# Kernel tuning notes

Measured on AMD Instinct MI355X. Metric: run time of the kernel, lower is better.

## Reference

```python
import jax, jax.numpy as jnp
import numpy as np

EPS = 1e-06

def elu_feature_map(x):
    return jax.nn.elu(x) + 1.0

def setup_inputs() -> dict:
    key = jax.random.key(0)
    kq, kk, kv = jax.random.split(key, 3)
    N, L, S, H, D = 8, 8192, 8192, 8, 32
    queries = jax.random.normal(kq, (N, L, H, D), dtype=jnp.float32)
    keys = jax.random.normal(kk, (N, S, H, D), dtype=jnp.float32)
    values = jax.random.normal(kv, (N, S, H, D), dtype=jnp.float32)
    return {"queries": queries, "keys": keys, "values": values}

def reference(queries, keys, values):
    # Linear attention: phi(Q) (phi(K)^T V) normalized by phi(Q) . sum(phi(K))
    Q = elu_feature_map(queries)            # [N, L, H, D]
    K = elu_feature_map(keys)               # [N, S, H, D]
    v_length = values.shape[1]
    v = values / v_length                   # [N, S, H, Dv]
    KV = jnp.einsum('nshd,nshv->nhdv', K, v)           # [N, H, D, Dv]
    Z = 1.0 / (jnp.einsum('nlhd,nhd->nlh', Q, K.sum(axis=1)) + EPS)  # [N, L, H]
    out = jnp.einsum('nlhd,nhdv->nlhv', Q, KV) * Z[..., None] * v_length
    return out
```

## Files before the change

kernel.cpp:

```cpp
#include <hip/hip_runtime.h>
#include <hip/hip_bf16.h>


#define N_      8
#define L_      8192
#define S_      8192
#define H_      8
#define D_      32
#define NH_     64
#define CH1_    16
#define SPC1_   512
#define STR1_   36
#define KVE_    (D_ * D_)
#define PKS_    (KVE_ + D_)

typedef short short8 __attribute__((ext_vector_type(8)));
typedef float f32x4  __attribute__((ext_vector_type(4)));

__device__ __forceinline__ float phi_f(float x) {
    return x > 0.f ? x + 1.f : __expf(x);
}

__device__ __forceinline__ unsigned short bf16_bits(float x) {
    __hip_bfloat16 h = __float2bfloat16(x);
    unsigned short u;
    __builtin_memcpy(&u, &h, 2);
    return u;
}

__device__ __forceinline__ void split_bf16(float x, short& hi, short& lo) {
    __hip_bfloat16 hb = __float2bfloat16(x);
    const float xh = __bfloat162float(hb);
    __hip_bfloat16 lb = __float2bfloat16(x - xh);
    __builtin_memcpy(&hi, &hb, 2);
    __builtin_memcpy(&lo, &lb, 2);
}

template <bool ATOMIC>
__global__ __launch_bounds__(256) void la_phase1(
    const float* __restrict__ keys, const float* __restrict__ values,
    float* __restrict__ outp )
{
    __shared__ unsigned kS[2][32][STR1_];
    __shared__ unsigned vS[2][32][STR1_];
    __shared__ float red_ks[4][8][4];
    const int nh = blockIdx.x, chunk = blockIdx.y;
    const int n = nh >> 3, h = nh & 7;
    const int t = threadIdx.x, lane = t & 63, w = t >> 6;
    const int row8 = t >> 3;
    const int c4   = t & 7;
    const int row_l = lane & 15, kg = lane >> 4;
    const int dt = w >> 1, vt = w & 1;
    const int odd = row8 & 1;
    const int dv0 = (c4 << 2) + (odd ? 2 : 0);
    const int s2lo = row8 >> 1;
    const float* kb = keys   + ((size_t)n * S_) * 256 + h * 32 + (c4 << 2);
    const float* vb = values + ((size_t)n * S_) * 256 + h * 32 + (c4 << 2);
    const int s0 = chunk * SPC1_;

    float ks4[4] = {0.f, 0.f, 0.f, 0.f};
    f32x4 cacc = {0.f, 0.f, 0.f, 0.f};
    float4 Lka, Lkb, Lva, Lvb;

    auto LOADT = [&](int tb) {
        const size_t g0 = ((size_t)(s0 + (tb << 6) + row8)) << 8;
        const size_t g1 = ((size_t)(s0 + (tb << 6) + row8 + 32)) << 8;
        Lka = *(const float4*)(kb + g0);
        Lkb = *(const float4*)(kb + g1);
        Lva = *(const float4*)(vb + g0);
        Lvb = *(const float4*)(vb + g1);
    };
    auto STORE4 = [&](unsigned (*Sarr)[STR1_], const unsigned short* x, int s2) {
        const unsigned mA = (unsigned)x[0] | ((unsigned)x[1] << 16);
        const unsigned mB = (unsigned)x[2] | ((unsigned)x[3] << 16);
        const unsigned pA = __shfl_xor(mA, 8);
        const unsigned pB = __shfl_xor(mB, 8);
        const unsigned m = odd ? mB : mA, p = odd ? pB : pA;
        const unsigned se = odd ? p : m;
        const unsigned so = odd ? m : p;
        const unsigned w0 = (se & 0xffffu) | ((so & 0xffffu) << 16);
        const unsigned w1 = (se >> 16) | (so & 0xffff0000u);
        Sarr[dv0][4 * ((s2 >> 2) ^ (dv0 >> 3)) + (s2 & 3)]           = w0;
        Sarr[dv0 + 1][4 * ((s2 >> 2) ^ ((dv0 + 1) >> 3)) + (s2 & 3)] = w1;
    };
    auto PROCT = [&](int buf) {
        const float f0[4] = {phi_f(Lka.x), phi_f(Lka.y), phi_f(Lka.z), phi_f(Lka.w)};
        const float f1[4] = {phi_f(Lkb.x), phi_f(Lkb.y), phi_f(Lkb.z), phi_f(Lkb.w)};
        unsigned short kx[4], ky[4], vx[4], vy[4];
#pragma unroll
        for (int j = 0; j < 4; ++j) ks4[j] += f0[j] + f1[j];
        kx[0] = bf16_bits(f0[0]); kx[1] = bf16_bits(f0[1]);
        kx[2] = bf16_bits(f0[2]); kx[3] = bf16_bits(f0[3]);
        ky[0] = bf16_bits(f1[0]); ky[1] = bf16_bits(f1[1]);
        ky[2] = bf16_bits(f1[2]); ky[3] = bf16_bits(f1[3]);
        vx[0] = bf16_bits(Lva.x); vx[1] = bf16_bits(Lva.y);
        vx[2] = bf16_bits(Lva.z); vx[3] = bf16_bits(Lva.w);
        vy[0] = bf16_bits(Lvb.x); vy[1] = bf16_bits(Lvb.y);
        vy[2] = bf16_bits(Lvb.z); vy[3] = bf16_bits(Lvb.w);
        STORE4(kS[buf], kx, s2lo);
        STORE4(kS[buf], ky, s2lo + 16);
        STORE4(vS[buf], vx, s2lo);
        STORE4(vS[buf], vy, s2lo + 16);
    };
    auto FRAG = [&](const unsigned (*Sarr)[STR1_], int row, int sh) -> short8 {
        const int g = ((sh << 2) | kg) ^ (row >> 3);
        union { uint4 u; short8 s; } U;
        U.u = *(const uint4*)&Sarr[row][g << 2];
        return U.s;
    };
    auto COMPT = [&](int buf) {
#pragma unroll
        for (int sh = 0; sh < 2; ++sh) {
            const short8 A = FRAG(kS[buf], (dt << 4) + row_l, sh);
            const short8 B = FRAG(vS[buf], (vt << 4) + row_l, sh);
            cacc = __builtin_amdgcn_mfma_f32_16x16x32_bf16(A, B, cacc, 0, 0, 0);
        }
    };

    LOADT(0);
    PROCT(0);
    __syncthreads();
#pragma unroll
    for (int tb = 0; tb < 8; ++tb) {
        const int cur = tb & 1;
        if (tb < 7) LOADT(tb + 1);
        COMPT(cur);
        if (tb < 7) PROCT(cur ^ 1);
        __syncthreads();
    }

#pragma unroll
    for (int j = 0; j < 4; ++j) {
        float x = ks4[j];
        x += __shfl_xor(x, 8);
        x += __shfl_xor(x, 16);
        x += __shfl_xor(x, 32);
        ks4[j] = x;
    }
    if (lane < 8) {
#pragma unroll
        for (int j = 0; j < 4; ++j) red_ks[w][lane][j] = ks4[j];
    }
    __syncthreads();

    if (ATOMIC) {
        float* p = outp + (size_t)nh * PKS_;
#pragma unroll
        for (int r = 0; r < 4; ++r) {
            const int dd = (dt << 4) + (kg << 2) + r;
            const int vv = (vt << 4) + row_l;
            atomicAdd(&p[dd * D_ + vv], cacc[r]);
        }
        if (t < 32) {
            const float s = red_ks[0][t >> 2][t & 3] + red_ks[1][t >> 2][t & 3]
                          + red_ks[2][t >> 2][t & 3] + red_ks[3][t >> 2][t & 3];
            atomicAdd(&p[KVE_ + t], s);
        }
    } else {
        float* p = outp + ((size_t)nh * CH1_ + chunk) * PKS_;
#pragma unroll
        for (int r = 0; r < 4; ++r) {
            const int dd = (dt << 4) + (kg << 2) + r;
            const int vv = (vt << 4) + row_l;
            p[dd * D_ + vv] = cacc[r];
        }
        if (t < 32) {
            p[KVE_ + t] = red_ks[0][t >> 2][t & 3] + red_ks[1][t >> 2][t & 3]
                        + red_ks[2][t >> 2][t & 3] + red_ks[3][t >> 2][t & 3];
        }
    }
}

__global__ __launch_bounds__(256) void la_reduce(
    const float* __restrict__ partials,
    short* __restrict__ kvThi, short* __restrict__ kvTlo,
    float* __restrict__ ksumf)
{
    const int nh = blockIdx.x;
    for (int e = threadIdx.x; e < PKS_; e += 256) {
        const float* p = partials + (size_t)nh * CH1_ * PKS_ + e;
        float s = 0.f;
#pragma unroll
        for (int c = 0; c < CH1_; ++c) s += p[(size_t)c * PKS_];
        if (e < KVE_) {
            const int d = e >> 5, v = e & 31;
            short hi, lo; split_bf16(s, hi, lo);
            kvThi[nh * KVE_ + v * D_ + d] = hi;
            kvTlo[nh * KVE_ + v * D_ + d] = lo;
        } else {
            ksumf[nh * D_ + (e - KVE_)] = s;
        }
    }
}

__global__ __launch_bounds__(256) void la_convert(
    const float* __restrict__ kvf,
    short* __restrict__ kvThi, short* __restrict__ kvTlo,
    float* __restrict__ ksumf)
{
    const int nh = blockIdx.x;
    for (int e = threadIdx.x; e < PKS_; e += 256) {
        const float s = kvf[(size_t)nh * PKS_ + e];
        if (e < KVE_) {
            const int d = e >> 5, v = e & 31;
            short hi, lo; split_bf16(s, hi, lo);
            kvThi[nh * KVE_ + v * D_ + d] = hi;
            kvTlo[nh * KVE_ + v * D_ + d] = lo;
        } else {
            ksumf[nh * D_ + (e - KVE_)] = s;
        }
    }
}

__global__ void la_zero(float* __restrict__ p, int nelem) {
    const int i = blockIdx.x * 256 + threadIdx.x;
    if (i < nelem) p[i] = 0.f;
}

__global__ __launch_bounds__(256) void la_phase2(
    const float* __restrict__ queries,
    const short* __restrict__ kvThi, const short* __restrict__ kvTlo,
    const float* __restrict__ ksumf, float* __restrict__ out)
{
    const int t = threadIdx.x, lane = t & 63, w = t >> 6;
    const int wt = blockIdx.x * 4 + w;
    const int h  = wt & 7;
    const int rt = wt >> 3;
    const size_t rowg0 = (size_t)rt * 16;
    const int n = (int)(rowg0 >> 13);
    const int nh = n * 8 + h;
    const int row_l = lane & 15;
    const int kg    = lane >> 4;

    const float* qp = queries + (rowg0 + row_l) * 256 + h * D_ + kg * 8;
    float qa[8];
    {
        const float4 qA = *(const float4*)(qp);
        const float4 qB = *(const float4*)(qp + 4);
        qa[0] = phi_f(qA.x); qa[1] = phi_f(qA.y); qa[2] = phi_f(qA.z); qa[3] = phi_f(qA.w);
        qa[4] = phi_f(qB.x); qa[5] = phi_f(qB.y); qa[6] = phi_f(qB.z); qa[7] = phi_f(qB.w);
    }
    short8 ahi, alo;
#pragma unroll
    for (int e = 0; e < 8; ++e) {
        short hs, ls; split_bf16(qa[e], hs, ls);
        ahi[e] = hs; alo[e] = ls;
    }

    const short* bh = kvThi + (size_t)nh * KVE_;
    const short* bl = kvTlo + (size_t)nh * KVE_;
    const short8 bh0 = *(const short8*)(bh + (row_l     ) * D_ + kg * 8);
    const short8 bh1 = *(const short8*)(bh + (row_l + 16) * D_ + kg * 8);
    const short8 bl0 = *(const short8*)(bl + (row_l     ) * D_ + kg * 8);
    const short8 bl1 = *(const short8*)(bl + (row_l + 16) * D_ + kg * 8);

    f32x4 c0 = {0.f, 0.f, 0.f, 0.f}, c1 = {0.f, 0.f, 0.f, 0.f};
    c0 = __builtin_amdgcn_mfma_f32_16x16x32_bf16(alo, bh0, c0, 0, 0, 0);
    c0 = __builtin_amdgcn_mfma_f32_16x16x32_bf16(ahi, bl0, c0, 0, 0, 0);
    c0 = __builtin_amdgcn_mfma_f32_16x16x32_bf16(ahi, bh0, c0, 0, 0, 0);
    c1 = __builtin_amdgcn_mfma_f32_16x16x32_bf16(alo, bh1, c1, 0, 0, 0);
    c1 = __builtin_amdgcn_mfma_f32_16x16x32_bf16(ahi, bl1, c1, 0, 0, 0);
    c1 = __builtin_amdgcn_mfma_f32_16x16x32_bf16(ahi, bh1, c1, 0, 0, 0);

    const float* ksp = ksumf + nh * D_ + kg * 8;
    float dt;
    {
        const float4 kA = *(const float4*)(ksp);
        const float4 kB = *(const float4*)(ksp + 4);
        dt = qa[0] * kA.x;
        dt = fmaf(qa[1], kA.y, dt); dt = fmaf(qa[2], kA.z, dt);
        dt = fmaf(qa[3], kA.w, dt); dt = fmaf(qa[4], kB.x, dt);
        dt = fmaf(qa[5], kB.y, dt); dt = fmaf(qa[6], kB.z, dt);
        dt = fmaf(qa[7], kB.w, dt);
    }
    dt += __shfl_xor(dt, 16);
    dt += __shfl_xor(dt, 32);

    float* ob = out + rowg0 * 256 + h * D_ + row_l;
#pragma unroll
    for (int r = 0; r < 4; ++r) {
        const int rowp = kg * 4 + r;
        const float drow = __shfl(dt, rowp);
        const float z = __builtin_amdgcn_rcpf(drow + 1e-6f);
        ob[(size_t)rowp * 256]      = c0[r] * z;
        ob[(size_t)rowp * 256 + 16] = c1[r] * z;
    }
}

extern "C" void kernel_launch(void* const* d_in, const int* in_sizes, int n_in,
                              void* d_out, int out_size, void* d_ws, size_t ws_size,
                              hipStream_t stream)
{
    const float* queries = (const float*)d_in[0];
    const float* keys    = (const float*)d_in[1];
    const float* values  = (const float*)d_in[2];
    float* out = (float*)d_out;
    float* ws  = (float*)d_ws;

    const size_t partial_elems = (size_t)NH_ * CH1_ * PKS_;
    const size_t split_elems   = (size_t)NH_ * KVE_;
    const size_t split_floats  = split_elems / 2;
    const size_t ksum_floats   = (size_t)NH_ * D_;
    const dim3 blk(256);
    const int p2_blocks = (N_ * L_ * H_) / 16 / 4;

    if (ws_size >= (partial_elems + 2 * split_floats + ksum_floats) * sizeof(float)) {
        float* partials = ws;
        short* kvThi = (short*)(ws + partial_elems);
        short* kvTlo = kvThi + split_elems;
        float* ksumf = (float*)(kvTlo + split_elems);
        la_phase1<false><<<dim3(NH_, CH1_), blk, 0, stream>>>(keys, values, partials);
        la_reduce<<<dim3(NH_), blk, 0, stream>>>(partials, kvThi, kvTlo, ksumf);
        la_phase2<<<dim3(p2_blocks), blk, 0, stream>>>(queries, kvThi, kvTlo, ksumf, out);
    } else {
        float* kvf = ws;
        short* kvThi = (short*)(ws + (size_t)NH_ * PKS_);
        short* kvTlo = kvThi + split_elems;
        float* ksumf = (float*)(kvTlo + split_elems);
        const int nz = (int)((size_t)NH_ * PKS_);
        la_zero<<<dim3((nz + 255) / 256), blk, 0, stream>>>(kvf, nz);
        la_phase1<true><<<dim3(NH_, CH1_), blk, 0, stream>>>(keys, values, kvf);
        la_convert<<<dim3(NH_), blk, 0, stream>>>(kvf, kvThi, kvTlo, ksumf);
        la_phase2<<<dim3(p2_blocks), blk, 0, stream>>>(queries, kvThi, kvTlo, ksumf, out);
    }
}
```

Before: 62.97 us.

## Process eight row tiles per wave in phase2, reusing KV fragments and prefetching queries

Phase 2 now gives each block a fixed (n,h) pair and makes each wave loop over eight 16-row tiles. The split-bf16 KV fragments and the key-sum are loaded once per wave and reused across those tiles. The next tile's query loads are issued before the current tile's MFMA and normalisation work, a software prefetch. The grid shrinks from 8192 blocks to 1024, which cuts launch and per-wave setup costs but lowers parallelism and could leave less latency hiding on the memory-bound output stores.

```diff
diff --git a/kernel.cpp b/kernel.cpp
--- a/kernel.cpp
+++ b/kernel.cpp
@@ -223,67 +223,71 @@
     const float* __restrict__ ksumf, float* __restrict__ out)
 {
     const int t = threadIdx.x, lane = t & 63, w = t >> 6;
-    const int wt = blockIdx.x * 4 + w;
-    const int h  = wt & 7;
-    const int rt = wt >> 3;
-    const size_t rowg0 = (size_t)rt * 16;
-    const int n = (int)(rowg0 >> 13);
-    const int nh = n * 8 + h;
+    const int bx = blockIdx.x;
+    const int nh = bx & 63;
+    const int g  = bx >> 6;
+    const int n = nh >> 3, h = nh & 7;
     const int row_l = lane & 15;
     const int kg    = lane >> 4;
 
-    const float* qp = queries + (rowg0 + row_l) * 256 + h * D_ + kg * 8;
-    float qa[8];
-    {
-        const float4 qA = *(const float4*)(qp);
-        const float4 qB = *(const float4*)(qp + 4);
-        qa[0] = phi_f(qA.x); qa[1] = phi_f(qA.y); qa[2] = phi_f(qA.z); qa[3] = phi_f(qA.w);
-        qa[4] = phi_f(qB.x); qa[5] = phi_f(qB.y); qa[6] = phi_f(qB.z); qa[7] = phi_f(qB.w);
-    }
-    short8 ahi, alo;
-#pragma unroll
-    for (int e = 0; e < 8; ++e) {
-        short hs, ls; split_bf16(qa[e], hs, ls);
-        ahi[e] = hs; alo[e] = ls;
-    }
-
-    const short* bh = kvThi + (size_t)nh * KVE_;
-    const short* bl = kvTlo + (size_t)nh * KVE_;
-    const short8 bh0 = *(const short8*)(bh + (row_l     ) * D_ + kg * 8);
-    const short8 bh1 = *(const short8*)(bh + (row_l + 16) * D_ + kg * 8);
-    const short8 bl0 = *(const short8*)(bl + (row_l     ) * D_ + kg * 8);
-    const short8 bl1 = *(const short8*)(bl + (row_l + 16) * D_ + kg * 8);
-
-    f32x4 c0 = {0.f, 0.f, 0.f, 0.f}, c1 = {0.f, 0.f, 0.f, 0.f};
-    c0 = __builtin_amdgcn_mfma_f32_16x16x32_bf16(alo, bh0, c0, 0, 0, 0);
-    c0 = __builtin_amdgcn_mfma_f32_16x16x32_bf16(ahi, bl0, c0, 0, 0, 0);
-    c0 = __builtin_amdgcn_mfma_f32_16x16x32_bf16(ahi, bh0, c0, 0, 0, 0);
-    c1 = __builtin_amdgcn_mfma_f32_16x16x32_bf16(alo, bh1, c1, 0, 0, 0);
-    c1 = __builtin_amdgcn_mfma_f32_16x16x32_bf16(ahi, bl1, c1, 0, 0, 0);
-    c1 = __builtin_amdgcn_mfma_f32_16x16x32_bf16(ahi, bh1, c1, 0, 0, 0);
-
-    const float* ksp = ksumf + nh * D_ + kg * 8;
-    float dt;
-    {
-        const float4 kA = *(const float4*)(ksp);
-        const float4 kB = *(const float4*)(ksp + 4);
-        dt = qa[0] * kA.x;
+    const short* bhp = kvThi + (size_t)nh * KVE_;
+    const short* blp = kvTlo + (size_t)nh * KVE_;
+    const short8 bh0 = *(const short8*)(bhp + (row_l     ) * D_ + kg * 8);
+    const short8 bh1 = *(const short8*)(bhp + (row_l + 16) * D_ + kg * 8);
+    const short8 bl0 = *(const short8*)(blp + (row_l     ) * D_ + kg * 8);
+    const short8 bl1 = *(const short8*)(blp + (row_l + 16) * D_ + kg * 8);
+    const float4 kA = *(const float4*)(ksumf + nh * D_ + kg * 8);
+    const float4 kB = *(const float4*)(ksumf + nh * D_ + kg * 8 + 4);
+
+    const size_t row0 = ((size_t)n << 13) + ((size_t)(g * 4 + w) << 7);
+    const float* qbase = queries + (row0 + row_l) * 256 + h * D_ + kg * 8;
+    float* obase = out + row0 * 256 + h * D_ + row_l;
+
+    float4 qA = *(const float4*)(qbase);
+    float4 qB = *(const float4*)(qbase + 4);
+
+#pragma unroll
+    for (int tt = 0; tt < 8; ++tt) {
+        const float4 cA = qA, cB = qB;
+        if (tt < 7) {
+            const float* qp = qbase + (size_t)(tt + 1) * 16 * 256;
+            qA = *(const float4*)(qp);
+            qB = *(const float4*)(qp + 4);
+        }
+        float qa[8];
+        qa[0] = phi_f(cA.x); qa[1] = phi_f(cA.y); qa[2] = phi_f(cA.z); qa[3] = phi_f(cA.w);
+        qa[4] = phi_f(cB.x); qa[5] = phi_f(cB.y); qa[6] = phi_f(cB.z); qa[7] = phi_f(cB.w);
+        short8 ahi, alo;
+#pragma unroll
+        for (int e = 0; e < 8; ++e) {
+            short hs, ls; split_bf16(qa[e], hs, ls);
+            ahi[e] = hs; alo[e] = ls;
+        }
+        f32x4 c0 = {0.f, 0.f, 0.f, 0.f}, c1 = {0.f, 0.f, 0.f, 0.f};
+        c0 = __builtin_amdgcn_mfma_f32_16x16x32_bf16(alo, bh0, c0, 0, 0, 0);
+        c0 = __builtin_amdgcn_mfma_f32_16x16x32_bf16(ahi, bl0, c0, 0, 0, 0);
+        c0 = __builtin_amdgcn_mfma_f32_16x16x32_bf16(ahi, bh0, c0, 0, 0, 0);
+        c1 = __builtin_amdgcn_mfma_f32_16x16x32_bf16(alo, bh1, c1, 0, 0, 0);
+        c1 = __builtin_amdgcn_mfma_f32_16x16x32_bf16(ahi, bl1, c1, 0, 0, 0);
+        c1 = __builtin_amdgcn_mfma_f32_16x16x32_bf16(ahi, bh1, c1, 0, 0, 0);
+
+        float dt = qa[0] * kA.x;
         dt = fmaf(qa[1], kA.y, dt); dt = fmaf(qa[2], kA.z, dt);
         dt = fmaf(qa[3], kA.w, dt); dt = fmaf(qa[4], kB.x, dt);
         dt = fmaf(qa[5], kB.y, dt); dt = fmaf(qa[6], kB.z, dt);
         dt = fmaf(qa[7], kB.w, dt);
-    }
-    dt += __shfl_xor(dt, 16);
-    dt += __shfl_xor(dt, 32);
-
-    float* ob = out + rowg0 * 256 + h * D_ + row_l;
-#pragma unroll
-    for (int r = 0; r < 4; ++r) {
-        const int rowp = kg * 4 + r;
-        const float drow = __shfl(dt, rowp);
-        const float z = __builtin_amdgcn_rcpf(drow + 1e-6f);
-        ob[(size_t)rowp * 256]      = c0[r] * z;
-        ob[(size_t)rowp * 256 + 16] = c1[r] * z;
+        dt += __shfl_xor(dt, 16);
+        dt += __shfl_xor(dt, 32);
+
+        float* ob = obase + (size_t)tt * 16 * 256;
+#pragma unroll
+        for (int r = 0; r < 4; ++r) {
+            const int rowp = kg * 4 + r;
+            const float drow = __shfl(dt, rowp);
+            const float z = __builtin_amdgcn_rcpf(drow + 1e-6f);
+            ob[(size_t)rowp * 256]      = c0[r] * z;
+            ob[(size_t)rowp * 256 + 16] = c1[r] * z;
+        }
     }
 }
 
@@ -302,7 +306,7 @@
     const size_t split_floats  = split_elems / 2;
     const size_t ksum_floats   = (size_t)NH_ * D_;
     const dim3 blk(256);
-    const int p2_blocks = (N_ * L_ * H_) / 16 / 4;
+    const int p2_blocks = 1024;
 
     if (ws_size >= (partial_elems + 2 * split_floats + ksum_floats) * sizeof(float)) {
         float* partials = ws;
```

After: 70.10 us. 11.3% more time.

## Process two row tiles per wave in phase2 and swizzle block order

Applied to the files above, without the earlier changes.

Each wave in la_phase2 now handles 32 query rows instead of 16. The KV bf16 split fragments and ksum are loaded once and reused across both row tiles, and both tiles' query loads are issued up front. The grid is halved, and a block-index swizzle remaps blocks across 8 groups, likely to spread neighbouring blocks over XCDs or L2. This cuts redundant KV loads and per-wave overhead, at the cost of half as many waves and more register pressure.

```diff
diff --git a/kernel.cpp b/kernel.cpp
--- a/kernel.cpp
+++ b/kernel.cpp
@@ -223,29 +223,18 @@
     const float* __restrict__ ksumf, float* __restrict__ out)
 {
     const int t = threadIdx.x, lane = t & 63, w = t >> 6;
-    const int wt = blockIdx.x * 4 + w;
-    const int h  = wt & 7;
-    const int rt = wt >> 3;
-    const size_t rowg0 = (size_t)rt * 16;
-    const int n = (int)(rowg0 >> 13);
+    const int bx0 = blockIdx.x;
+    const int px  = bx0 >> 1;
+    const int swz = (px & 7) * 256 + (px >> 3);
+    const int bx  = (swz << 1) | (bx0 & 1);
+    const int wt  = bx * 4 + w;
+    const int h   = wt & 7;
+    const int rt2 = wt >> 3;
+    const size_t rowg0 = (size_t)rt2 * 32;
+    const int n  = (int)(rowg0 >> 13);
     const int nh = n * 8 + h;
     const int row_l = lane & 15;
     const int kg    = lane >> 4;
-
-    const float* qp = queries + (rowg0 + row_l) * 256 + h * D_ + kg * 8;
-    float qa[8];
-    {
-        const float4 qA = *(const float4*)(qp);
-        const float4 qB = *(const float4*)(qp + 4);
-        qa[0] = phi_f(qA.x); qa[1] = phi_f(qA.y); qa[2] = phi_f(qA.z); qa[3] = phi_f(qA.w);
-        qa[4] = phi_f(qB.x); qa[5] = phi_f(qB.y); qa[6] = phi_f(qB.z); qa[7] = phi_f(qB.w);
-    }
-    short8 ahi, alo;
-#pragma unroll
-    for (int e = 0; e < 8; ++e) {
-        short hs, ls; split_bf16(qa[e], hs, ls);
-        ahi[e] = hs; alo[e] = ls;
-    }
 
     const short* bh = kvThi + (size_t)nh * KVE_;
     const short* bl = kvTlo + (size_t)nh * KVE_;
@@ -253,37 +242,57 @@
     const short8 bh1 = *(const short8*)(bh + (row_l + 16) * D_ + kg * 8);
     const short8 bl0 = *(const short8*)(bl + (row_l     ) * D_ + kg * 8);
     const short8 bl1 = *(const short8*)(bl + (row_l + 16) * D_ + kg * 8);
-
-    f32x4 c0 = {0.f, 0.f, 0.f, 0.f}, c1 = {0.f, 0.f, 0.f, 0.f};
-    c0 = __builtin_amdgcn_mfma_f32_16x16x32_bf16(alo, bh0, c0, 0, 0, 0);
-    c0 = __builtin_amdgcn_mfma_f32_16x16x32_bf16(ahi, bl0, c0, 0, 0, 0);
-    c0 = __builtin_amdgcn_mfma_f32_16x16x32_bf16(ahi, bh0, c0, 0, 0, 0);
-    c1 = __builtin_amdgcn_mfma_f32_16x16x32_bf16(alo, bh1, c1, 0, 0, 0);
-    c1 = __builtin_amdgcn_mfma_f32_16x16x32_bf16(ahi, bl1, c1, 0, 0, 0);
-    c1 = __builtin_amdgcn_mfma_f32_16x16x32_bf16(ahi, bh1, c1, 0, 0, 0);
-
-    const float* ksp = ksumf + nh * D_ + kg * 8;
-    float dt;
-    {
-        const float4 kA = *(const float4*)(ksp);
-        const float4 kB = *(const float4*)(ksp + 4);
-        dt = qa[0] * kA.x;
+    const float4 kA = *(const float4*)(ksumf + nh * D_ + kg * 8);
+    const float4 kB = *(const float4*)(ksumf + nh * D_ + kg * 8 + 4);
+
+    const float* qp0 = queries + (rowg0 + row_l) * 256 + h * D_ + kg * 8;
+    const float* qp1 = qp0 + 16 * 256;
+    float4 qA[2], qB[2];
+    qA[0] = *(const float4*)(qp0);
+    qB[0] = *(const float4*)(qp0 + 4);
+    qA[1] = *(const float4*)(qp1);
+    qB[1] = *(const float4*)(qp1 + 4);
+
+    float* ob0 = out + rowg0 * 256 + h * D_ + row_l;
+
+#pragma unroll
+    for (int tt = 0; tt < 2; ++tt) {
+        float qa[8];
+        qa[0] = phi_f(qA[tt].x); qa[1] = phi_f(qA[tt].y);
+        qa[2] = phi_f(qA[tt].z); qa[3] = phi_f(qA[tt].w);
+        qa[4] = phi_f(qB[tt].x); qa[5] = phi_f(qB[tt].y);
+        qa[6] = phi_f(qB[tt].z); qa[7] = phi_f(qB[tt].w);
+        short8 ahi, alo;
+#pragma unroll
+        for (int e = 0; e < 8; ++e) {
+            short hs, ls; split_bf16(qa[e], hs, ls);
+            ahi[e] = hs; alo[e] = ls;
+        }
+        f32x4 c0 = {0.f, 0.f, 0.f, 0.f}, c1 = {0.f, 0.f, 0.f, 0.f};
+        c0 = __builtin_amdgcn_mfma_f32_16x16x32_bf16(alo, bh0, c0, 0, 0, 0);
+        c0 = __builtin_amdgcn_mfma_f32_16x16x32_bf16(ahi, bl0, c0, 0, 0, 0);
+        c0 = __builtin_amdgcn_mfma_f32_16x16x32_bf16(ahi, bh0, c0, 0, 0, 0);
+        c1 = __builtin_amdgcn_mfma_f32_16x16x32_bf16(alo, bh1, c1, 0, 0, 0);
+        c1 = __builtin_amdgcn_mfma_f32_16x16x32_bf16(ahi, bl1, c1, 0, 0, 0);
+        c1 = __builtin_amdgcn_mfma_f32_16x16x32_bf16(ahi, bh1, c1, 0, 0, 0);
+
+        float dt = qa[0] * kA.x;
         dt = fmaf(qa[1], kA.y, dt); dt = fmaf(qa[2], kA.z, dt);
         dt = fmaf(qa[3], kA.w, dt); dt = fmaf(qa[4], kB.x, dt);
         dt = fmaf(qa[5], kB.y, dt); dt = fmaf(qa[6], kB.z, dt);
         dt = fmaf(qa[7], kB.w, dt);
-    }
-    dt += __shfl_xor(dt, 16);
-    dt += __shfl_xor(dt, 32);
-
-    float* ob = out + rowg0 * 256 + h * D_ + row_l;
-#pragma unroll
-    for (int r = 0; r < 4; ++r) {
-        const int rowp = kg * 4 + r;
-        const float drow = __shfl(dt, rowp);
-        const float z = __builtin_amdgcn_rcpf(drow + 1e-6f);
-        ob[(size_t)rowp * 256]      = c0[r] * z;
-        ob[(size_t)rowp * 256 + 16] = c1[r] * z;
+        dt += __shfl_xor(dt, 16);
+        dt += __shfl_xor(dt, 32);
+
+        float* ob = ob0 + (size_t)tt * 16 * 256;
+#pragma unroll
+        for (int r = 0; r < 4; ++r) {
+            const int rowp = kg * 4 + r;
+            const float drow = __shfl(dt, rowp);
+            const float z = __builtin_amdgcn_rcpf(drow + 1e-6f);
+            ob[(size_t)rowp * 256]      = c0[r] * z;
+            ob[(size_t)rowp * 256 + 16] = c1[r] * z;
+        }
     }
 }
 
@@ -302,7 +311,7 @@
     const size_t split_floats  = split_elems / 2;
     const size_t ksum_floats   = (size_t)NH_ * D_;
     const dim3 blk(256);
-    const int p2_blocks = (N_ * L_ * H_) / 16 / 4;
+    const int p2_blocks = (N_ * L_ * H_) / 32 / 4;
 
     if (ws_size >= (partial_elems + 2 * split_floats + ksum_floats) * sizeof(float)) {
         float* partials = ws;
```

Measured after the change: 66.75 us. 1.06x slower.

## Stage phase-2 query rows through swizzled LDS with 512-thread blocks

Applied to the files above, without the earlier changes.

Phase 2 now uses one 512-thread block per 16 rows, one wave per head. Each block loads the full 16x256 query rows into shared memory with coalesced float4 reads, applying phi on the way and an XOR swizzle to avoid bank conflicts. Each wave then reads its head slice from LDS. This replaces the earlier strided per-wave 32-byte global reads with fully contiguous row loads, at the cost of 16KB of LDS per block and a block barrier.

```diff
diff --git a/kernel.cpp b/kernel.cpp
--- a/kernel.cpp
+++ b/kernel.cpp
@@ -217,34 +217,31 @@
     if (i < nelem) p[i] = 0.f;
 }
 
-__global__ __launch_bounds__(256) void la_phase2(
+__global__ __launch_bounds__(512) void la_phase2(
     const float* __restrict__ queries,
     const short* __restrict__ kvThi, const short* __restrict__ kvTlo,
     const float* __restrict__ ksumf, float* __restrict__ out)
 {
+    __shared__ float qs[16 * 256];
     const int t = threadIdx.x, lane = t & 63, w = t >> 6;
-    const int wt = blockIdx.x * 4 + w;
-    const int h  = wt & 7;
-    const int rt = wt >> 3;
-    const size_t rowg0 = (size_t)rt * 16;
-    const int n = (int)(rowg0 >> 13);
+    const size_t rowg0 = (size_t)blockIdx.x * 16;
+    const int n  = (int)(rowg0 >> 13);
+    const int h  = w;
     const int nh = n * 8 + h;
     const int row_l = lane & 15;
     const int kg    = lane >> 4;
 
-    const float* qp = queries + (rowg0 + row_l) * 256 + h * D_ + kg * 8;
-    float qa[8];
     {
-        const float4 qA = *(const float4*)(qp);
-        const float4 qB = *(const float4*)(qp + 4);
-        qa[0] = phi_f(qA.x); qa[1] = phi_f(qA.y); qa[2] = phi_f(qA.z); qa[3] = phi_f(qA.w);
-        qa[4] = phi_f(qB.x); qa[5] = phi_f(qB.y); qa[6] = phi_f(qB.z); qa[7] = phi_f(qB.w);
-    }
-    short8 ahi, alo;
-#pragma unroll
-    for (int e = 0; e < 8; ++e) {
-        short hs, ls; split_bf16(qa[e], hs, ls);
-        ahi[e] = hs; alo[e] = ls;
+        const int row = t & 15, seg = t >> 4;
+        const float* qp = queries + (rowg0 + row) * 256 + seg * 8;
+        const float4 a = *(const float4*)(qp);
+        const float4 b = *(const float4*)(qp + 4);
+        const int p0 = ((seg << 1) | 0) ^ (row & 7);
+        const int p1 = ((seg << 1) | 1) ^ (row & 7);
+        *(float4*)&qs[row * 256 + p0 * 4] =
+            make_float4(phi_f(a.x), phi_f(a.y), phi_f(a.z), phi_f(a.w));
+        *(float4*)&qs[row * 256 + p1 * 4] =
+            make_float4(phi_f(b.x), phi_f(b.y), phi_f(b.z), phi_f(b.w));
     }
 
     const short* bh = kvThi + (size_t)nh * KVE_;
@@ -253,6 +250,26 @@
     const short8 bh1 = *(const short8*)(bh + (row_l + 16) * D_ + kg * 8);
     const short8 bl0 = *(const short8*)(bl + (row_l     ) * D_ + kg * 8);
     const short8 bl1 = *(const short8*)(bl + (row_l + 16) * D_ + kg * 8);
+    const float4 kA = *(const float4*)(ksumf + nh * D_ + kg * 8);
+    const float4 kB = *(const float4*)(ksumf + nh * D_ + kg * 8 + 4);
+
+    __syncthreads();
+
+    float qa[8];
+    {
+        const int g0 = (h * 8 + kg * 2)     ^ (row_l & 7);
+        const int g1 = (h * 8 + kg * 2 + 1) ^ (row_l & 7);
+        const float4 f0 = *(const float4*)&qs[row_l * 256 + g0 * 4];
+        const float4 f1 = *(const float4*)&qs[row_l * 256 + g1 * 4];
+        qa[0] = f0.x; qa[1] = f0.y; qa[2] = f0.z; qa[3] = f0.w;
+        qa[4] = f1.x; qa[5] = f1.y; qa[6] = f1.z; qa[7] = f1.w;
+    }
+    short8 ahi, alo;
+#pragma unroll
+    for (int e = 0; e < 8; ++e) {
+        short hs, ls; split_bf16(qa[e], hs, ls);
+        ahi[e] = hs; alo[e] = ls;
+    }
 
     f32x4 c0 = {0.f, 0.f, 0.f, 0.f}, c1 = {0.f, 0.f, 0.f, 0.f};
     c0 = __builtin_amdgcn_mfma_f32_16x16x32_bf16(alo, bh0, c0, 0, 0, 0);
@@ -262,17 +279,11 @@
     c1 = __builtin_amdgcn_mfma_f32_16x16x32_bf16(ahi, bl1, c1, 0, 0, 0);
     c1 = __builtin_amdgcn_mfma_f32_16x16x32_bf16(ahi, bh1, c1, 0, 0, 0);
 
-    const float* ksp = ksumf + nh * D_ + kg * 8;
-    float dt;
-    {
-        const float4 kA = *(const float4*)(ksp);
-        const float4 kB = *(const float4*)(ksp + 4);
-        dt = qa[0] * kA.x;
-        dt = fmaf(qa[1], kA.y, dt); dt = fmaf(qa[2], kA.z, dt);
-        dt = fmaf(qa[3], kA.w, dt); dt = fmaf(qa[4], kB.x, dt);
-        dt = fmaf(qa[5], kB.y, dt); dt = fmaf(qa[6], kB.z, dt);
-        dt = fmaf(qa[7], kB.w, dt);
-    }
+    float dt = qa[0] * kA.x;
+    dt = fmaf(qa[1], kA.y, dt); dt = fmaf(qa[2], kA.z, dt);
+    dt = fmaf(qa[3], kA.w, dt); dt = fmaf(qa[4], kB.x, dt);
+    dt = fmaf(qa[5], kB.y, dt); dt = fmaf(qa[6], kB.z, dt);
+    dt = fmaf(qa[7], kB.w, dt);
     dt += __shfl_xor(dt, 16);
     dt += __shfl_xor(dt, 32);
 
@@ -302,7 +313,8 @@
     const size_t split_floats  = split_elems / 2;
     const size_t ksum_floats   = (size_t)NH_ * D_;
     const dim3 blk(256);
-    const int p2_blocks = (N_ * L_ * H_) / 16 / 4;
+    const dim3 blk2(512);
+    const int p2_blocks = (N_ * L_) / 16;
 
     if (ws_size >= (partial_elems + 2 * split_floats + ksum_floats) * sizeof(float)) {
         float* partials = ws;
@@ -311,7 +323,7 @@
         float* ksumf = (float*)(kvTlo + split_elems);
         la_phase1<false><<<dim3(NH_, CH1_), blk, 0, stream>>>(keys, values, partials);
         la_reduce<<<dim3(NH_), blk, 0, stream>>>(partials, kvThi, kvTlo, ksumf);
-        la_phase2<<<dim3(p2_blocks), blk, 0, stream>>>(queries, kvThi, kvTlo, ksumf, out);
+        la_phase2<<<dim3(p2_blocks), blk2, 0, stream>>>(queries, kvThi, kvTlo, ksumf, out);
     } else {
         float* kvf = ws;
         short* kvThi = (short*)(ws + (size_t)NH_ * PKS_);
@@ -321,6 +333,6 @@
         la_zero<<<dim3((nz + 255) / 256), blk, 0, stream>>>(kvf, nz);
         la_phase1<true><<<dim3(NH_, CH1_), blk, 0, stream>>>(keys, values, kvf);
         la_convert<<<dim3(NH_), blk, 0, stream>>>(kvf, kvThi, kvTlo, ksumf);
-        la_phase2<<<dim3(p2_blocks), blk, 0, stream>>>(queries, kvThi, kvTlo, ksumf, out);
-    }
-}
+        la_phase2<<<dim3(p2_blocks), blk2, 0, stream>>>(queries, kvThi, kvTlo, ksumf, out);
+    }
+}
```

Result: no change. 62.92 us (-0.1%).
